# Kernel tuning notes

Hardware: AMD Instinct MI355X
Metric: run time of the kernel (lower is better)

The kernel has to match this reference:

```python
import jax, jax.numpy as jnp
import numpy as np

N = 128          # number of nodes (particles)
NR = N * (N - 1) # number of directed edges, receiver-major order
B = 128          # batch
C = 16           # channel dim


def setup_inputs() -> dict:
    key = jax.random.key(0)
    x = jax.random.normal(key, (B, NR, C), dtype=jnp.float32)
    # assign_matrices enumerates (r, s) pairs receiver-major, so edge i has
    # receiver i // (N-1); Rr2 is the one-hot indicator of this mapping.
    receivers = jnp.arange(NR, dtype=jnp.int32) // (N - 1)
    return {"x": x, "receivers": receivers}


def reference(x, receivers):
    # exp of edge scores
    e = jnp.exp(x)  # [B, Nr, C]
    # tensordot(exp, Rr2, axes=[1,1]) == segment-sum over edges grouped by receiver
    seg = jax.ops.segment_sum(e.transpose(1, 0, 2), receivers, num_segments=N)  # [N, B, C]
    # tensordot(exp_sum, Rr2, axes=1) == gather each edge's receiver sum back to edges
    denom = seg[receivers]                 # [Nr, B, C]
    denom = denom.transpose(1, 2, 0)       # [B, C, Nr]
    # NOTE: the original divides the raw inputs (not exp) by the summed exp
    return x.transpose(0, 2, 1) / denom    # [B, C, Nr]
```

## Files before the change

kernel.cpp:

```cpp
#include <hip/hip_runtime.h>

#define N_NODES 128
#define NE      127
#define BATCH   128
#define CH      16
#define NRE     (N_NODES * NE)
#define LDSS    132

__global__ __launch_bounds__(256) void attn2_kernel(const float* __restrict__ x,
                                                    float* __restrict__ out) {
    __shared__ float tile[CH * LDSS];
    __shared__ float partial[16 * CH];
    __shared__ float rdenom[CH];

    const int t   = threadIdx.x;
    const int blk = blockIdx.x;
    const int b   = blk >> 7;
    const int r   = blk & (N_NODES - 1);

    const float4* xseg = (const float4*)(x + (size_t)(b * NRE + r * NE) * CH);

    #pragma unroll
    for (int it = 0; it < 2; ++it) {
        int f = t + it * 256;
        if (f < 508) {
            float4 v = xseg[f];
            int edge = f >> 2;
            int p    = (f & 3) << 2;
            tile[(p + 0) * LDSS + edge] = v.x;
            tile[(p + 1) * LDSS + edge] = v.y;
            tile[(p + 2) * LDSS + edge] = v.z;
            tile[(p + 3) * LDSS + edge] = v.w;
        }
    }
    __syncthreads();

    {
        const int c     = t & 15;
        const int chunk = t >> 4;
        float s = 0.f;
        #pragma unroll
        for (int m = 0; m < 8; ++m) {
            int local = chunk + (m << 4);
            if (local < NE) s += __expf(tile[c * LDSS + local]);
        }
        partial[chunk * 16 + c] = s;
    }
    __syncthreads();

    if (t < 16) {
        float s = 0.f;
        #pragma unroll
        for (int ch = 0; ch < 16; ++ch) s += partial[ch * 16 + t];
        rdenom[t] = 1.0f / s;
    }
    __syncthreads();

    float* oseg = out + (size_t)b * CH * NRE + (size_t)r * NE;
    #pragma unroll
    for (int it = 0; it < 8; ++it) {
        int e = t + it * 256;
        if (e < CH * NE) {
            int c     = e / NE;
            int local = e - c * NE;
            oseg[(size_t)c * NRE + local] = tile[c * LDSS + local] * rdenom[c];
        }
    }
}

extern "C" void kernel_launch(void* const* d_in, const int* in_sizes, int n_in,
                              void* d_out, int out_size, void* d_ws, size_t ws_size,
                              hipStream_t stream) {
    const float* x = (const float*)d_in[0];
    float* out = (float*)d_out;
    attn2_kernel<<<BATCH * N_NODES, 256, 0, stream>>>(x, out);
}
```

Baseline: 245.1 us.

## Assign one wavefront per receiver segment with shuffle-reduced exp sums

Each 64-thread wavefront now owns one (batch, receiver) segment, and each block packs four segments. The exp sums are accumulated in registers during the load and reduced with wave shuffles, which removes the partial-sum shared buffer and two block barriers. The reciprocal denominator is kept in a spare tile column. The integer division in the store loop is replaced by incremental index tracking, and stores use nontemporal hints. Each thread now does more iterations, and the tile stride of 128 may cause LDS bank conflicts on the transposed writes.

New measurement: 251.2 us. 2.5% more time.

```diff
diff --git a/kernel.cpp b/kernel.cpp
--- a/kernel.cpp
+++ b/kernel.cpp
@@ -1,70 +1,69 @@
 #include <hip/hip_runtime.h>
 
-#define N_NODES 128
-#define NE      127
-#define BATCH   128
-#define CH      16
-#define NRE     (N_NODES * NE)
-#define LDSS    132
+#define NN   128
+#define NE   127
+#define CH   16
+#define NRE  (NN * NE)
+#define STR  128
 
-__global__ __launch_bounds__(256) void attn2_kernel(const float* __restrict__ x,
-                                                    float* __restrict__ out) {
-    __shared__ float tile[CH * LDSS];
-    __shared__ float partial[16 * CH];
-    __shared__ float rdenom[CH];
+__global__ __launch_bounds__(256, 5) void attn2_kernel(const float* __restrict__ x,
+                                                       float* __restrict__ out) {
+    __shared__ float tile[4][CH * STR];
 
-    const int t   = threadIdx.x;
-    const int blk = blockIdx.x;
-    const int b   = blk >> 7;
-    const int r   = blk & (N_NODES - 1);
+    const int t   = threadIdx.x & 63;
+    const int w   = threadIdx.x >> 6;
+    const int seg = (blockIdx.x << 2) | w;
+    const int b   = seg >> 7;
+    const int r   = seg & (NN - 1);
 
-    const float4* xseg = (const float4*)(x + (size_t)(b * NRE + r * NE) * CH);
+    float* T = tile[w];
+
+    const float4* xseg = (const float4*)(x + (size_t)seg * NE * CH);
+    const int p  = (t & 3) << 2;
+    const int er = t >> 2;
+
+    float a0 = 0.f, a1 = 0.f, a2 = 0.f, a3 = 0.f;
+    #pragma unroll
+    for (int it = 0; it < 8; ++it) {
+        int f = t + (it << 6);
+        if (f < 508) {
+            float4 v = xseg[f];
+            int edge = er + (it << 4);
+            T[(p + 0) * STR + edge] = v.x;
+            T[(p + 1) * STR + edge] = v.y;
+            T[(p + 2) * STR + edge] = v.z;
+            T[(p + 3) * STR + edge] = v.w;
+            a0 += __expf(v.x); a1 += __expf(v.y);
+            a2 += __expf(v.z); a3 += __expf(v.w);
+        }
+    }
 
     #pragma unroll
-    for (int it = 0; it < 2; ++it) {
-        int f = t + it * 256;
-        if (f < 508) {
-            float4 v = xseg[f];
-            int edge = f >> 2;
-            int p    = (f & 3) << 2;
-            tile[(p + 0) * LDSS + edge] = v.x;
-            tile[(p + 1) * LDSS + edge] = v.y;
-            tile[(p + 2) * LDSS + edge] = v.z;
-            tile[(p + 3) * LDSS + edge] = v.w;
-        }
+    for (int m = 4; m <= 32; m <<= 1) {
+        a0 += __shfl_xor(a0, m, 64);
+        a1 += __shfl_xor(a1, m, 64);
+        a2 += __shfl_xor(a2, m, 64);
+        a3 += __shfl_xor(a3, m, 64);
     }
-    __syncthreads();
-
-    {
-        const int c     = t & 15;
-        const int chunk = t >> 4;
-        float s = 0.f;
-        #pragma unroll
-        for (int m = 0; m < 8; ++m) {
-            int local = chunk + (m << 4);
-            if (local < NE) s += __expf(tile[c * LDSS + local]);
-        }
-        partial[chunk * 16 + c] = s;
-    }
-    __syncthreads();
-
-    if (t < 16) {
-        float s = 0.f;
-        #pragma unroll
-        for (int ch = 0; ch < 16; ++ch) s += partial[ch * 16 + t];
-        rdenom[t] = 1.0f / s;
+    if (t < 4) {
+        T[(p + 0) * STR + NE] = 1.0f / a0;
+        T[(p + 1) * STR + NE] = 1.0f / a1;
+        T[(p + 2) * STR + NE] = 1.0f / a2;
+        T[(p + 3) * STR + NE] = 1.0f / a3;
     }
     __syncthreads();
 
     float* oseg = out + (size_t)b * CH * NRE + (size_t)r * NE;
-    #pragma unroll
-    for (int it = 0; it < 8; ++it) {
-        int e = t + it * 256;
-        if (e < CH * NE) {
-            int c     = e / NE;
-            int local = e - c * NE;
-            oseg[(size_t)c * NRE + local] = tile[c * LDSS + local] * rdenom[c];
+    int c = 0, local = t;
+    #pragma unroll 8
+    for (int it = 0; it < 32; ++it) {
+        if (c < CH) {
+            float v  = T[c * STR + local];
+            float rd = T[c * STR + NE];
+            __builtin_nontemporal_store(v * rd, oseg + c * NRE + local);
         }
+        local += 64;
+        if (local >= NE) { local -= NE; ++c; }
     }
 }
 
@@ -73,5 +72,5 @@
                               hipStream_t stream) {
     const float* x = (const float*)d_in[0];
     float* out = (float*)d_out;
-    attn2_kernel<<<BATCH * N_NODES, 256, 0, stream>>>(x, out);
+    attn2_kernel<<<(128 * 128) / 4, 256, 0, stream>>>(x, out);
 }
```
